# Kernel tuning notes

Hardware: AMD Instinct MI355X
Metric: run time of the kernel (lower is better)

## Reference

```python
import jax, jax.numpy as jnp
import numpy as np

NUM_NODES = 100000
NUM_EDGES = 625000
IN_FEATURES = 128
OUT_FEATURES = 128


def setup_inputs() -> dict:
    key = jax.random.key(0)
    k1, k2, k3, k4 = jax.random.split(key, 4)
    x = jax.random.normal(k1, (NUM_NODES, IN_FEATURES), dtype=jnp.float32)
    edge_index = jax.random.randint(k2, (2, NUM_EDGES), 0, NUM_NODES, dtype=jnp.int64)
    # Xavier uniform for W (fan_in=IN, fan_out=OUT); B initialized to zeros in the
    # original, but we use small random values so gradients flow through both paths.
    limit = float(np.sqrt(6.0 / (IN_FEATURES + OUT_FEATURES)))
    W = jax.random.uniform(k3, (OUT_FEATURES, IN_FEATURES), dtype=jnp.float32,
                           minval=-limit, maxval=limit)
    B = jax.random.uniform(k4, (OUT_FEATURES, IN_FEATURES), dtype=jnp.float32,
                           minval=-limit, maxval=limit)
    return {"x": x, "edge_index": edge_index, "W": W, "B": B}


def reference(x, edge_index, W, B):
    sources, destinations = edge_index[0], edge_index[1]
    # message: gather destination features, scatter-add into source slots
    messages = x[destinations]                                        # [E, F_in]
    agg = jax.ops.segment_sum(messages, sources, num_segments=x.shape[0])  # [N, F_in]
    # in-degree (w.r.t. sources) normalization; zero-degree -> divide by 1
    deg = jax.ops.segment_sum(jnp.ones((sources.shape[0],), dtype=x.dtype),
                              sources, num_segments=x.shape[0])       # [N]
    deg = jnp.where(deg == 0, jnp.ones_like(deg), deg)
    agg = agg / deg[:, None]
    # update: (W @ messages.T + B @ x.T).T == messages @ W.T + x @ B.T
    out = agg @ W.T + x @ B.T                                         # [N, F_out]
    return out
```

## Files before the change

kernel.cpp:

```cpp
#include <hip/hip_runtime.h>

#define F_IN   128
#define F_OUT  128

typedef __attribute__((ext_vector_type(8))) short short8;
typedef __attribute__((ext_vector_type(4))) float floatx4;

__device__ __forceinline__ float bf16u_to_f_lo(unsigned int u) {
    union { unsigned int i; float f; } c; c.i = u << 16; return c.f;
}
__device__ __forceinline__ float bf16u_to_f_hi(unsigned int u) {
    union { unsigned int i; float f; } c; c.i = u & 0xffff0000u; return c.f;
}
__device__ __forceinline__ unsigned short f_to_bf16(float f) {
    union { float f; unsigned int i; } c; c.f = f;
    unsigned int u = c.i;
    u += 0x7fffu + ((u >> 16) & 1u);
    return (unsigned short)(u >> 16);
}
__device__ __forceinline__ unsigned int pack2(unsigned short a, unsigned short b) {
    return (unsigned int)a | ((unsigned int)b << 16);
}
__device__ __forceinline__ void acc8(float* a, uint4 v) {
    a[0] += bf16u_to_f_lo(v.x); a[1] += bf16u_to_f_hi(v.x);
    a[2] += bf16u_to_f_lo(v.y); a[3] += bf16u_to_f_hi(v.y);
    a[4] += bf16u_to_f_lo(v.z); a[5] += bf16u_to_f_hi(v.z);
    a[6] += bf16u_to_f_lo(v.w); a[7] += bf16u_to_f_hi(v.w);
}

__global__ __launch_bounds__(256) void prep_kernel(const float* __restrict__ x,
                                                   int* __restrict__ off,
                                                   unsigned short* __restrict__ xb, int N) {
    long tid = (long)blockIdx.x * blockDim.x + threadIdx.x;
    long nconv = (long)N * 32;
    long total = nconv + N;
    long stride = (long)gridDim.x * blockDim.x;
    for (; tid < total; tid += stride) {
        if (tid < nconv) {
            int row = (int)(tid >> 5);
            int seg = (int)(tid & 31);
            float4 v = *(const float4*)(x + (size_t)row * 128 + seg * 4);
            *(ushort4*)(xb + (size_t)row * 128 + seg * 4) =
                make_ushort4(f_to_bf16(v.x), f_to_bf16(v.y), f_to_bf16(v.z), f_to_bf16(v.w));
        } else {
            off[tid - nconv] = 0;
        }
    }
}

__global__ void hist_kernel(const int* __restrict__ src, int* __restrict__ cnt, int E) {
    int e = blockIdx.x * blockDim.x + threadIdx.x;
    if (e < E) atomicAdd(&cnt[src[e]], 1);
}

__global__ __launch_bounds__(256) void chunk_sums_kernel(const int* __restrict__ cnt,
                                                         int* __restrict__ partials, int n) {
    __shared__ int s[256];
    int b = blockIdx.x, t = threadIdx.x;
    int base = b * 1024 + t * 4;
    int sum = 0;
#pragma unroll
    for (int j = 0; j < 4; ++j) {
        int i = base + j;
        if (i < n) sum += cnt[i];
    }
    s[t] = sum;
    __syncthreads();
    for (int d = 128; d > 0; d >>= 1) {
        if (t < d) s[t] += s[t + d];
        __syncthreads();
    }
    if (t == 0) partials[b] = s[0];
}

__global__ __launch_bounds__(128) void scan_partials_kernel(const int* __restrict__ partials,
                                                            int* __restrict__ chunk_off, int nch) {
    __shared__ int s[128];
    int t = threadIdx.x;
    s[t] = (t < nch) ? partials[t] : 0;
    __syncthreads();
    for (int d = 1; d < 128; d <<= 1) {
        int val = s[t];
        int add = (t >= d) ? s[t - d] : 0;
        __syncthreads();
        s[t] = val + add;
        __syncthreads();
    }
    if (t < nch) chunk_off[t] = (t > 0) ? s[t - 1] : 0;
}

__global__ __launch_bounds__(256) void scan_chunks_kernel(int* __restrict__ off,
                                                          const int* __restrict__ chunk_off,
                                                          int n) {
    __shared__ int s[256];
    int b = blockIdx.x, t = threadIdx.x;
    int base = b * 1024 + t * 4;
    int v[4];
#pragma unroll
    for (int j = 0; j < 4; ++j) {
        int i = base + j;
        v[j] = (i < n) ? off[i] : 0;
    }
    int l1 = v[0], l2 = l1 + v[1], l3 = l2 + v[2], tot = l3 + v[3];
    s[t] = tot;
    __syncthreads();
    for (int d = 1; d < 256; d <<= 1) {
        int val = s[t];
        int add = (t >= d) ? s[t - d] : 0;
        __syncthreads();
        s[t] = val + add;
        __syncthreads();
    }
    int thr_excl = ((t > 0) ? s[t - 1] : 0) + chunk_off[b];
    if (base + 0 < n) off[base + 0] = thr_excl;
    if (base + 1 < n) off[base + 1] = thr_excl + l1;
    if (base + 2 < n) off[base + 2] = thr_excl + l2;
    if (base + 3 < n) off[base + 3] = thr_excl + l3;
}

__global__ void fill_kernel(const int* __restrict__ ei, int* __restrict__ off,
                            int* __restrict__ dst_sorted, int E) {
    int e = blockIdx.x * blockDim.x + threadIdx.x;
    if (e < E) {
        int s = ei[e];
        int d = ei[E + e];
        int p = atomicAdd(&off[s], 1);
        dst_sorted[p] = d;
    }
}

__global__ __launch_bounds__(256) void gather_gemm_kernel(const float* __restrict__ W,
                                                          const float* __restrict__ Bm,
                                                          const int* __restrict__ off,
                                                          const int* __restrict__ dst_sorted,
                                                          const unsigned short* __restrict__ xb,
                                                          float* __restrict__ out, int N) {
    __shared__ uint4 Bs[4096];
    int t = threadIdx.x;
    int lane = t & 63;
    int w = t >> 6;
    int m16 = lane & 15;
    int quad = lane >> 4;

#pragma unroll
    for (int nt2 = 0; nt2 < 2; ++nt2) {
        int nt = w * 2 + nt2;
        int n = nt * 16 + m16;
#pragma unroll
        for (int s = 0; s < 8; ++s) {
            int kbase = s * 32 + quad * 8;
            const float* srcp = (kbase < 128) ? (W + n * 128 + kbase)
                                              : (Bm + n * 128 + (kbase - 128));
            float4 v0 = *(const float4*)srcp;
            float4 v1 = *(const float4*)(srcp + 4);
            uint4 pk;
            pk.x = pack2(f_to_bf16(v0.x), f_to_bf16(v0.y));
            pk.y = pack2(f_to_bf16(v0.z), f_to_bf16(v0.w));
            pk.z = pack2(f_to_bf16(v1.x), f_to_bf16(v1.y));
            pk.w = pack2(f_to_bf16(v1.z), f_to_bf16(v1.w));
            Bs[(nt * 8 + s) * 64 + lane] = pk;
        }
    }
    __syncthreads();

    int rowbase = blockIdx.x * 128 + w * 32;
    short8 afrag[2][8];

#pragma unroll
    for (int g = 0; g < 2; ++g) {
        int node = rowbase + g * 16 + m16;
        if (node > N - 1) node = N - 1;
        int start = (node == 0) ? 0 : off[node - 1];
        int end = off[node];
        int deg = end - start;

        float acc[4][8];
#pragma unroll
        for (int s = 0; s < 4; ++s)
#pragma unroll
            for (int j = 0; j < 8; ++j) acc[s][j] = 0.0f;

        int j = start;
        for (; j + 2 <= end; j += 2) {
            int d0 = dst_sorted[j];
            int d1 = dst_sorted[j + 1];
            const char* p0 = (const char*)xb + (size_t)d0 * 256 + quad * 16;
            const char* p1 = (const char*)xb + (size_t)d1 * 256 + quad * 16;
            uint4 a0 = *(const uint4*)(p0);
            uint4 a1 = *(const uint4*)(p0 + 64);
            uint4 a2 = *(const uint4*)(p0 + 128);
            uint4 a3 = *(const uint4*)(p0 + 192);
            uint4 b0 = *(const uint4*)(p1);
            uint4 b1 = *(const uint4*)(p1 + 64);
            uint4 b2 = *(const uint4*)(p1 + 128);
            uint4 b3 = *(const uint4*)(p1 + 192);
            acc8(acc[0], a0); acc8(acc[1], a1); acc8(acc[2], a2); acc8(acc[3], a3);
            acc8(acc[0], b0); acc8(acc[1], b1); acc8(acc[2], b2); acc8(acc[3], b3);
        }
        if (j < end) {
            int d0 = dst_sorted[j];
            const char* p0 = (const char*)xb + (size_t)d0 * 256 + quad * 16;
            uint4 a0 = *(const uint4*)(p0);
            uint4 a1 = *(const uint4*)(p0 + 64);
            uint4 a2 = *(const uint4*)(p0 + 128);
            uint4 a3 = *(const uint4*)(p0 + 192);
            acc8(acc[0], a0); acc8(acc[1], a1); acc8(acc[2], a2); acc8(acc[3], a3);
        }

        float scale = (deg > 0) ? (1.0f / (float)deg) : 1.0f;
#pragma unroll
        for (int s = 0; s < 4; ++s) {
            uint4 pk;
            pk.x = pack2(f_to_bf16(acc[s][0] * scale), f_to_bf16(acc[s][1] * scale));
            pk.y = pack2(f_to_bf16(acc[s][2] * scale), f_to_bf16(acc[s][3] * scale));
            pk.z = pack2(f_to_bf16(acc[s][4] * scale), f_to_bf16(acc[s][5] * scale));
            pk.w = pack2(f_to_bf16(acc[s][6] * scale), f_to_bf16(acc[s][7] * scale));
            afrag[g][s] = *(short8*)&pk;
        }
        const char* q0 = (const char*)xb + (size_t)node * 256 + quad * 16;
#pragma unroll
        for (int s = 0; s < 4; ++s)
            afrag[g][4 + s] = *(const short8*)(q0 + s * 64);
    }

    floatx4 acc[2][8];
#pragma unroll
    for (int g = 0; g < 2; ++g)
#pragma unroll
        for (int nt = 0; nt < 8; ++nt) acc[g][nt] = (floatx4){0.f, 0.f, 0.f, 0.f};

#pragma unroll
    for (int nt = 0; nt < 8; ++nt) {
#pragma unroll
        for (int s = 0; s < 8; ++s) {
            short8 bfrag = *(const short8*)&Bs[(nt * 8 + s) * 64 + lane];
            acc[0][nt] = __builtin_amdgcn_mfma_f32_16x16x32_bf16(afrag[0][s], bfrag, acc[0][nt], 0, 0, 0);
            acc[1][nt] = __builtin_amdgcn_mfma_f32_16x16x32_bf16(afrag[1][s], bfrag, acc[1][nt], 0, 0, 0);
        }
    }

#pragma unroll
    for (int g = 0; g < 2; ++g)
#pragma unroll
        for (int nt = 0; nt < 8; ++nt)
#pragma unroll
            for (int r = 0; r < 4; ++r) {
                int gr = rowbase + g * 16 + quad * 4 + r;
                if (gr < N) out[(size_t)gr * 128 + nt * 16 + m16] = acc[g][nt][r];
            }
}

__global__ void zero_kernel(int* __restrict__ p, long n) {
    long i = (long)blockIdx.x * blockDim.x + threadIdx.x;
    long stride = (long)gridDim.x * blockDim.x;
    for (; i < n; i += stride) p[i] = 0;
}

__global__ __launch_bounds__(256) void convert_x_kernel(const float* __restrict__ x,
                                                        char* __restrict__ outb, int N) {
    long tid = (long)blockIdx.x * blockDim.x + threadIdx.x;
    if (tid >= (long)N * 32) return;
    int row = (int)(tid >> 5);
    int seg = (int)(tid & 31);
    float4 v = *(const float4*)(x + (size_t)row * 128 + seg * 4);
    *(ushort4*)(outb + (size_t)row * 512 + 256 + seg * 8) =
        make_ushort4(f_to_bf16(v.x), f_to_bf16(v.y), f_to_bf16(v.z), f_to_bf16(v.w));
}

__global__ __launch_bounds__(256) void gather_bf16_kernel(const int* __restrict__ off,
                                                          const int* __restrict__ dst_sorted,
                                                          char* __restrict__ outb, int N) {
    int node = blockIdx.x * 16 + (threadIdx.x >> 4);
    int lane = threadIdx.x & 15;
    if (node >= N) return;
    int start = (node == 0) ? 0 : off[node - 1];
    int end = off[node];
    float acc[8];
#pragma unroll
    for (int i = 0; i < 8; ++i) acc[i] = 0.0f;
    const char* xb = outb;
    int j = start;
    for (; j + 2 <= end; j += 2) {
        int d0 = dst_sorted[j];
        int d1 = dst_sorted[j + 1];
        uint4 a = *(const uint4*)(xb + (size_t)d0 * 512 + 256 + lane * 16);
        uint4 b = *(const uint4*)(xb + (size_t)d1 * 512 + 256 + lane * 16);
        acc8(acc, a); acc8(acc, b);
    }
    if (j < end) {
        int d0 = dst_sorted[j];
        uint4 a = *(const uint4*)(xb + (size_t)d0 * 512 + 256 + lane * 16);
        acc8(acc, a);
    }
    int deg = end - start;
    float scale = (deg > 0) ? (1.0f / (float)deg) : 1.0f;
    uint4 pk;
    pk.x = pack2(f_to_bf16(acc[0] * scale), f_to_bf16(acc[1] * scale));
    pk.y = pack2(f_to_bf16(acc[2] * scale), f_to_bf16(acc[3] * scale));
    pk.z = pack2(f_to_bf16(acc[4] * scale), f_to_bf16(acc[5] * scale));
    pk.w = pack2(f_to_bf16(acc[6] * scale), f_to_bf16(acc[7] * scale));
    *(uint4*)(outb + (size_t)node * 512 + lane * 16) = pk;
}

__global__ __launch_bounds__(256) void gemm_mfma_kernel(const float* __restrict__ W,
                                                        const float* __restrict__ Bm,
                                                        float* __restrict__ out, int N) {
    __shared__ uint4 Bs[4096];
    int t = threadIdx.x;
    int lane = t & 63;
    int w = t >> 6;
    int m16 = lane & 15;
    int quad = lane >> 4;
#pragma unroll
    for (int nt2 = 0; nt2 < 2; ++nt2) {
        int nt = w * 2 + nt2;
        int n = nt * 16 + m16;
#pragma unroll
        for (int s = 0; s < 8; ++s) {
            int kbase = s * 32 + quad * 8;
            const float* srcp = (kbase < 128) ? (W + n * 128 + kbase)
                                              : (Bm + n * 128 + (kbase - 128));
            float4 v0 = *(const float4*)srcp;
            float4 v1 = *(const float4*)(srcp + 4);
            uint4 pk;
            pk.x = pack2(f_to_bf16(v0.x), f_to_bf16(v0.y));
            pk.y = pack2(f_to_bf16(v0.z), f_to_bf16(v0.w));
            pk.z = pack2(f_to_bf16(v1.x), f_to_bf16(v1.y));
            pk.w = pack2(f_to_bf16(v1.z), f_to_bf16(v1.w));
            Bs[(nt * 8 + s) * 64 + lane] = pk;
        }
    }
    __syncthreads();

    int rowbase = blockIdx.x * 128 + w * 32;
    short8 afrag[2][8];
#pragma unroll
    for (int g = 0; g < 2; ++g) {
        int arow = rowbase + g * 16 + m16;
        if (arow > N - 1) arow = N - 1;
        const char* ab = (const char*)out + (size_t)arow * 512;
#pragma unroll
        for (int s = 0; s < 8; ++s)
            afrag[g][s] = *(const short8*)(ab + s * 64 + quad * 16);
    }

    floatx4 acc[2][8];
#pragma unroll
    for (int g = 0; g < 2; ++g)
#pragma unroll
        for (int nt = 0; nt < 8; ++nt) acc[g][nt] = (floatx4){0.f, 0.f, 0.f, 0.f};

#pragma unroll
    for (int nt = 0; nt < 8; ++nt) {
#pragma unroll
        for (int s = 0; s < 8; ++s) {
            short8 bfrag = *(const short8*)&Bs[(nt * 8 + s) * 64 + lane];
            acc[0][nt] = __builtin_amdgcn_mfma_f32_16x16x32_bf16(afrag[0][s], bfrag, acc[0][nt], 0, 0, 0);
            acc[1][nt] = __builtin_amdgcn_mfma_f32_16x16x32_bf16(afrag[1][s], bfrag, acc[1][nt], 0, 0, 0);
        }
    }
#pragma unroll
    for (int g = 0; g < 2; ++g)
#pragma unroll
        for (int nt = 0; nt < 8; ++nt)
#pragma unroll
            for (int r = 0; r < 4; ++r) {
                int gr = rowbase + g * 16 + quad * 4 + r;
                if (gr < N) out[(size_t)gr * 128 + nt * 16 + m16] = acc[g][nt][r];
            }
}


extern "C" void kernel_launch(void* const* d_in, const int* in_sizes, int n_in,
                              void* d_out, int out_size, void* d_ws, size_t ws_size,
                              hipStream_t stream) {
    const float* x = (const float*)d_in[0];
    const int* ei = (const int*)d_in[1];
    const float* W = (const float*)d_in[2];
    const float* Bm = (const float*)d_in[3];
    float* out = (float*)d_out;

    const int N = in_sizes[0] / F_IN;
    const int E = in_sizes[1] / 2;
    const int NCHUNK = (N + 1023) / 1024;

    int* off        = (int*)d_ws;
    int* partials   = off + N;
    int* chunk_off  = partials + 128;
    int* dst_sorted = chunk_off + 128;
    size_t xb_off   = (((size_t)(N + 256 + E) * sizeof(int)) + 255) & ~(size_t)255;
    unsigned short* xb = (unsigned short*)((char*)d_ws + xb_off);

    const size_t need_fused = xb_off + (size_t)N * 128 * sizeof(unsigned short);
    const size_t need_csr   = ((size_t)N + 256 + (size_t)E) * sizeof(int);

    if (ws_size >= need_fused) {
        prep_kernel<<<512, 256, 0, stream>>>(x, off, xb, N);
        hist_kernel<<<(E + 255) / 256, 256, 0, stream>>>(ei, off, E);
        chunk_sums_kernel<<<NCHUNK, 256, 0, stream>>>(off, partials, N);
        scan_partials_kernel<<<1, 128, 0, stream>>>(partials, chunk_off, NCHUNK);
        scan_chunks_kernel<<<NCHUNK, 256, 0, stream>>>(off, chunk_off, N);
        fill_kernel<<<(E + 255) / 256, 256, 0, stream>>>(ei, off, dst_sorted, E);
        gather_gemm_kernel<<<(N + 127) / 128, 256, 0, stream>>>(W, Bm, off, dst_sorted, xb, out, N);
    } else if (ws_size >= need_csr) {
        zero_kernel<<<256, 256, 0, stream>>>(off, N);
        hist_kernel<<<(E + 255) / 256, 256, 0, stream>>>(ei, off, E);
        chunk_sums_kernel<<<NCHUNK, 256, 0, stream>>>(off, partials, N);
        scan_partials_kernel<<<1, 128, 0, stream>>>(partials, chunk_off, NCHUNK);
        scan_chunks_kernel<<<NCHUNK, 256, 0, stream>>>(off, chunk_off, N);
        fill_kernel<<<(E + 255) / 256, 256, 0, stream>>>(ei, off, dst_sorted, E);
        {
            long tot = (long)N * 32;
            convert_x_kernel<<<(int)((tot + 255) / 256), 256, 0, stream>>>(x, (char*)out, N);
        }
        gather_bf16_kernel<<<(N + 15) / 16, 256, 0, stream>>>(off, dst_sorted, (char*)out, N);
        gemm_mfma_kernel<<<(N + 127) / 128, 256, 0, stream>>>(W, Bm, out, N);
    }
}
```

Measured before the change: 238.5 us.

## Use decoupled look-back scan and split GEMM into two K-halves to cut LDS

Replaces the three-kernel prefix scan with a single-pass decoupled look-back scan that uses flagged 64-bit state words, removing two kernel launches. The look-back state is zeroed inside the prep kernel. The gather-GEMM kernel now stages only W in LDS, runs the aggregated half of the MFMA, then reloads the LDS buffer with B and runs the self-feature half. This halves shared memory and the live A-fragment registers, aiming at higher occupancy, at the cost of an extra barrier and serialized staging. The look-back spin relies on blocks being scheduled in order for forward progress.

```diff
diff --git a/kernel.cpp b/kernel.cpp
--- a/kernel.cpp
+++ b/kernel.cpp
@@ -5,6 +5,7 @@
 
 typedef __attribute__((ext_vector_type(8))) short short8;
 typedef __attribute__((ext_vector_type(4))) float floatx4;
+typedef unsigned long long ull;
 
 __device__ __forceinline__ float bf16u_to_f_lo(unsigned int u) {
     union { unsigned int i; float f; } c; c.i = u << 16; return c.f;
@@ -33,7 +34,7 @@
                                                    unsigned short* __restrict__ xb, int N) {
     long tid = (long)blockIdx.x * blockDim.x + threadIdx.x;
     long nconv = (long)N * 32;
-    long total = nconv + N;
+    long total = nconv + N + 256;
     long stride = (long)gridDim.x * blockDim.x;
     for (; tid < total; tid += stride) {
         if (tid < nconv) {
@@ -53,46 +54,12 @@
     if (e < E) atomicAdd(&cnt[src[e]], 1);
 }
 
-__global__ __launch_bounds__(256) void chunk_sums_kernel(const int* __restrict__ cnt,
-                                                         int* __restrict__ partials, int n) {
+#define FLG_AGG  (1ULL << 62)
+#define FLG_INC  (2ULL << 62)
+__global__ __launch_bounds__(256) void scan_lookback_kernel(int* __restrict__ off,
+                                                            ull* __restrict__ state, int n) {
     __shared__ int s[256];
-    int b = blockIdx.x, t = threadIdx.x;
-    int base = b * 1024 + t * 4;
-    int sum = 0;
-#pragma unroll
-    for (int j = 0; j < 4; ++j) {
-        int i = base + j;
-        if (i < n) sum += cnt[i];
-    }
-    s[t] = sum;
-    __syncthreads();
-    for (int d = 128; d > 0; d >>= 1) {
-        if (t < d) s[t] += s[t + d];
-        __syncthreads();
-    }
-    if (t == 0) partials[b] = s[0];
-}
-
-__global__ __launch_bounds__(128) void scan_partials_kernel(const int* __restrict__ partials,
-                                                            int* __restrict__ chunk_off, int nch) {
-    __shared__ int s[128];
-    int t = threadIdx.x;
-    s[t] = (t < nch) ? partials[t] : 0;
-    __syncthreads();
-    for (int d = 1; d < 128; d <<= 1) {
-        int val = s[t];
-        int add = (t >= d) ? s[t - d] : 0;
-        __syncthreads();
-        s[t] = val + add;
-        __syncthreads();
-    }
-    if (t < nch) chunk_off[t] = (t > 0) ? s[t - 1] : 0;
-}
-
-__global__ __launch_bounds__(256) void scan_chunks_kernel(int* __restrict__ off,
-                                                          const int* __restrict__ chunk_off,
-                                                          int n) {
-    __shared__ int s[256];
+    __shared__ int s_excl;
     int b = blockIdx.x, t = threadIdx.x;
     int base = b * 1024 + t * 4;
     int v[4];
@@ -111,7 +78,32 @@
         s[t] = val + add;
         __syncthreads();
     }
-    int thr_excl = ((t > 0) ? s[t - 1] : 0) + chunk_off[b];
+    int chunk_sum = s[255];
+    if (t == 0) {
+        if (b == 0) {
+            atomicExch(&state[0], FLG_INC | (unsigned int)chunk_sum);
+            s_excl = 0;
+        } else {
+            atomicExch(&state[b], FLG_AGG | (unsigned int)chunk_sum);
+        }
+    }
+    __syncthreads();
+    if (b > 0 && t == 0) {
+        int running = 0;
+        int i = b - 1;
+        while (true) {
+            ull st = atomicAdd(&state[i], 0ULL);
+            ull flg = st & (3ULL << 62);
+            if (flg == 0) continue;
+            running += (int)(unsigned int)st;
+            if (flg == FLG_INC) break;
+            --i;
+        }
+        atomicExch(&state[b], FLG_INC | (unsigned int)(running + chunk_sum));
+        s_excl = running;
+    }
+    __syncthreads();
+    int thr_excl = ((t > 0) ? s[t - 1] : 0) + s_excl;
     if (base + 0 < n) off[base + 0] = thr_excl;
     if (base + 1 < n) off[base + 1] = thr_excl + l1;
     if (base + 2 < n) off[base + 2] = thr_excl + l2;
@@ -135,7 +127,7 @@
                                                           const int* __restrict__ dst_sorted,
                                                           const unsigned short* __restrict__ xb,
                                                           float* __restrict__ out, int N) {
-    __shared__ uint4 Bs[4096];
+    __shared__ uint4 Bs[2048];
     int t = threadIdx.x;
     int lane = t & 63;
     int w = t >> 6;
@@ -147,10 +139,8 @@
         int nt = w * 2 + nt2;
         int n = nt * 16 + m16;
 #pragma unroll
-        for (int s = 0; s < 8; ++s) {
-            int kbase = s * 32 + quad * 8;
-            const float* srcp = (kbase < 128) ? (W + n * 128 + kbase)
-                                              : (Bm + n * 128 + (kbase - 128));
+        for (int s = 0; s < 4; ++s) {
+            const float* srcp = W + n * 128 + s * 32 + quad * 8;
             float4 v0 = *(const float4*)srcp;
             float4 v1 = *(const float4*)(srcp + 4);
             uint4 pk;
@@ -158,18 +148,20 @@
             pk.y = pack2(f_to_bf16(v0.z), f_to_bf16(v0.w));
             pk.z = pack2(f_to_bf16(v1.x), f_to_bf16(v1.y));
             pk.w = pack2(f_to_bf16(v1.z), f_to_bf16(v1.w));
-            Bs[(nt * 8 + s) * 64 + lane] = pk;
+            Bs[(nt * 4 + s) * 64 + lane] = pk;
         }
     }
     __syncthreads();
 
     int rowbase = blockIdx.x * 128 + w * 32;
-    short8 afrag[2][8];
+    int node_g[2];
+    short8 afrag[2][4];
 
 #pragma unroll
     for (int g = 0; g < 2; ++g) {
         int node = rowbase + g * 16 + m16;
         if (node > N - 1) node = N - 1;
+        node_g[g] = node;
         int start = (node == 0) ? 0 : off[node - 1];
         int end = off[node];
         int deg = end - start;
@@ -217,23 +209,57 @@
             pk.w = pack2(f_to_bf16(acc[s][6] * scale), f_to_bf16(acc[s][7] * scale));
             afrag[g][s] = *(short8*)&pk;
         }
-        const char* q0 = (const char*)xb + (size_t)node * 256 + quad * 16;
+    }
+
+    floatx4 acc[2][8];
+#pragma unroll
+    for (int g = 0; g < 2; ++g)
+#pragma unroll
+        for (int nt = 0; nt < 8; ++nt) acc[g][nt] = (floatx4){0.f, 0.f, 0.f, 0.f};
+
+#pragma unroll
+    for (int nt = 0; nt < 8; ++nt) {
+#pragma unroll
+        for (int s = 0; s < 4; ++s) {
+            short8 bfrag = *(const short8*)&Bs[(nt * 4 + s) * 64 + lane];
+            acc[0][nt] = __builtin_amdgcn_mfma_f32_16x16x32_bf16(afrag[0][s], bfrag, acc[0][nt], 0, 0, 0);
+            acc[1][nt] = __builtin_amdgcn_mfma_f32_16x16x32_bf16(afrag[1][s], bfrag, acc[1][nt], 0, 0, 0);
+        }
+    }
+    __syncthreads();
+
+#pragma unroll
+    for (int nt2 = 0; nt2 < 2; ++nt2) {
+        int nt = w * 2 + nt2;
+        int n = nt * 16 + m16;
+#pragma unroll
+        for (int s = 0; s < 4; ++s) {
+            const float* srcp = Bm + n * 128 + s * 32 + quad * 8;
+            float4 v0 = *(const float4*)srcp;
+            float4 v1 = *(const float4*)(srcp + 4);
+            uint4 pk;
+            pk.x = pack2(f_to_bf16(v0.x), f_to_bf16(v0.y));
+            pk.y = pack2(f_to_bf16(v0.z), f_to_bf16(v0.w));
+            pk.z = pack2(f_to_bf16(v1.x), f_to_bf16(v1.y));
+            pk.w = pack2(f_to_bf16(v1.z), f_to_bf16(v1.w));
+            Bs[(nt * 4 + s) * 64 + lane] = pk;
+        }
+    }
+    __syncthreads();
+
+#pragma unroll
+    for (int g = 0; g < 2; ++g) {
+        const char* q0 = (const char*)xb + (size_t)node_g[g] * 256 + quad * 16;
 #pragma unroll
         for (int s = 0; s < 4; ++s)
-            afrag[g][4 + s] = *(const short8*)(q0 + s * 64);
-    }
-
-    floatx4 acc[2][8];
-#pragma unroll
-    for (int g = 0; g < 2; ++g)
-#pragma unroll
-        for (int nt = 0; nt < 8; ++nt) acc[g][nt] = (floatx4){0.f, 0.f, 0.f, 0.f};
+            afrag[g][s] = *(const short8*)(q0 + s * 64);
+    }
 
 #pragma unroll
     for (int nt = 0; nt < 8; ++nt) {
 #pragma unroll
-        for (int s = 0; s < 8; ++s) {
-            short8 bfrag = *(const short8*)&Bs[(nt * 8 + s) * 64 + lane];
+        for (int s = 0; s < 4; ++s) {
+            short8 bfrag = *(const short8*)&Bs[(nt * 4 + s) * 64 + lane];
             acc[0][nt] = __builtin_amdgcn_mfma_f32_16x16x32_bf16(afrag[0][s], bfrag, acc[0][nt], 0, 0, 0);
             acc[1][nt] = __builtin_amdgcn_mfma_f32_16x16x32_bf16(afrag[1][s], bfrag, acc[1][nt], 0, 0, 0);
         }
@@ -385,9 +411,8 @@
     const int NCHUNK = (N + 1023) / 1024;
 
     int* off        = (int*)d_ws;
-    int* partials   = off + N;
-    int* chunk_off  = partials + 128;
-    int* dst_sorted = chunk_off + 128;
+    ull* state      = (ull*)(off + N);
+    int* dst_sorted = off + N + 256;
     size_t xb_off   = (((size_t)(N + 256 + E) * sizeof(int)) + 255) & ~(size_t)255;
     unsigned short* xb = (unsigned short*)((char*)d_ws + xb_off);
 
@@ -397,17 +422,13 @@
     if (ws_size >= need_fused) {
         prep_kernel<<<512, 256, 0, stream>>>(x, off, xb, N);
         hist_kernel<<<(E + 255) / 256, 256, 0, stream>>>(ei, off, E);
-        chunk_sums_kernel<<<NCHUNK, 256, 0, stream>>>(off, partials, N);
-        scan_partials_kernel<<<1, 128, 0, stream>>>(partials, chunk_off, NCHUNK);
-        scan_chunks_kernel<<<NCHUNK, 256, 0, stream>>>(off, chunk_off, N);
+        scan_lookback_kernel<<<NCHUNK, 256, 0, stream>>>(off, state, N);
         fill_kernel<<<(E + 255) / 256, 256, 0, stream>>>(ei, off, dst_sorted, E);
         gather_gemm_kernel<<<(N + 127) / 128, 256, 0, stream>>>(W, Bm, off, dst_sorted, xb, out, N);
     } else if (ws_size >= need_csr) {
-        zero_kernel<<<256, 256, 0, stream>>>(off, N);
+        zero_kernel<<<256, 256, 0, stream>>>(off, N + 256);
         hist_kernel<<<(E + 255) / 256, 256, 0, stream>>>(ei, off, E);
-        chunk_sums_kernel<<<NCHUNK, 256, 0, stream>>>(off, partials, N);
-        scan_partials_kernel<<<1, 128, 0, stream>>>(partials, chunk_off, NCHUNK);
-        scan_chunks_kernel<<<NCHUNK, 256, 0, stream>>>(off, chunk_off, N);
+        scan_lookback_kernel<<<NCHUNK, 256, 0, stream>>>(off, state, N);
         fill_kernel<<<(E + 255) / 256, 256, 0, stream>>>(ei, off, dst_sorted, E);
         {
             long tot = (long)N * 32;
```

Measured after the change: 252.5 us. 1.06x slower.
